# Kernel optimization log

Hardware: AMD Instinct MI355X
Metric: run time of the kernel (lower is better)

The kernel has to match this reference:

```python
import jax, jax.numpy as jnp
import numpy as np

VOCAB = 50265
D = 768
N_NEW = 200          # rows in new_embedding before zero-pad row
N_NODES = N_NEW - 1  # GAT operates on new_emb[1:-1]
N_EDGES = 1024
B, S = 8, 4096
LEAKY_SLOPE = 0.2


def setup_inputs() -> dict:
    key = jax.random.key(0)
    ks = jax.random.split(key, 7)
    x = jax.random.randint(ks[0], (B, S), 0, VOCAB + N_NEW, dtype=jnp.int32)
    orig_emb = jax.random.normal(ks[1], (VOCAB, D), dtype=jnp.float32) * 0.02
    new_emb = jax.random.normal(ks[2], (N_NEW + 1, D), dtype=jnp.float32) * 0.02
    new_emb = new_emb.at[0].set(0.0)  # prepended zero/pad row, as in __init__
    W = jax.random.normal(ks[3], (D, D), dtype=jnp.float32) * (1.0 / np.sqrt(D))
    a_src = jax.random.normal(ks[4], (D,), dtype=jnp.float32) * 0.1
    a_dst = jax.random.normal(ks[5], (D,), dtype=jnp.float32) * 0.1
    edge_index = jax.random.randint(ks[6], (2, N_EDGES), 0, N_NODES, dtype=jnp.int32)
    return {"x": x, "orig_emb": orig_emb, "new_emb": new_emb, "W": W,
            "a_src": a_src, "a_dst": a_dst, "edge_index": edge_index}


def _gat(feats, W, a_src, a_dst, edge_index):
    # Single-layer GAT over the label graph (edge list form, no dense NxN).
    h = feats @ W                                   # [N, D]
    src, dst = edge_index[0], edge_index[1]
    e = jax.nn.leaky_relu(h[src] @ a_src + h[dst] @ a_dst, LEAKY_SLOPE)  # [E]
    m = jax.ops.segment_max(e, dst, num_segments=N_NODES)               # stable softmax
    ex = jnp.exp(e - m[dst])
    denom = jax.ops.segment_sum(ex, dst, num_segments=N_NODES)
    alpha = ex / jnp.maximum(denom[dst], 1e-9)                          # [E]
    agg = jax.ops.segment_sum(alpha[:, None] * h[src], dst, num_segments=N_NODES)
    return jax.nn.elu(agg) + feats                  # residual, [N, D]


def reference(x, orig_emb, new_emb, W, a_src, a_dst, edge_index):
    # weight(): graph-encode new rows 1:-1, re-append last row, concat with vocab table
    node_feats = new_emb[1:-1]                      # [N_NODES, D]
    graph_feats = _gat(node_feats, W, a_src, a_dst, edge_index)
    table = jnp.concatenate([orig_emb, graph_feats, new_emb[-1:]], axis=0)  # [VOCAB+N_NEW, D]
    # F.embedding(x, table, padding_idx) forward is a plain gather
    return table[x]                                 # [B, S, D]
```

## Files before the change

kernel.cpp:

```cpp
#include <hip/hip_runtime.h>
#include <math.h>

#define VOCAB   50265
#define D       768
#define N_NEW   200
#define N_NODES 199
#define N_EDGES 1024
#define LEAKY   0.2f

typedef float f4 __attribute__((ext_vector_type(4)));

#define ROW_T 4
#define KC    8
#define KLEN  96
#define NROWT 50
#define NCH   (KC * 3)
#define NB_GEMM (NROWT * 3 * KC)

__global__ __launch_bounds__(256) void hybrid_kernel(
    const int* __restrict__ x, const float* __restrict__ orig_emb,
    const float* __restrict__ new_emb, const float* __restrict__ W,
    const float* __restrict__ a_src, const float* __restrict__ a_dst,
    float* __restrict__ partial, float* __restrict__ svp, float* __restrict__ dvp,
    float* __restrict__ out, int* __restrict__ gcnt, int* __restrict__ glist,
    int ntok)
{
    const int tid = threadIdx.x;
    const int bid = blockIdx.x;

    if (bid < NB_GEMM) {
        __shared__ float fts[ROW_T][KLEN];
        __shared__ float rS[ROW_T][4], rD[ROW_T][4];
        const int rowt = bid % NROWT;
        const int colt = (bid / NROWT) % 3;
        const int kc   = bid / (NROWT * 3);
        const int row0 = rowt * ROW_T;
        const int col  = colt * 256 + tid;
        const int k0   = kc * KLEN;
        const int lane = tid & 63, wid = tid >> 6;

        for (int i = tid; i < ROW_T * KLEN; i += 256) {
            int r  = i / KLEN;
            int kk = i - r * KLEN;
            int row = row0 + r;
            fts[r][kk] = (row < N_NODES) ? new_emb[(size_t)(1 + row) * D + k0 + kk] : 0.f;
        }
        __syncthreads();

        float acc[ROW_T] = {0.f, 0.f, 0.f, 0.f};
        #pragma unroll 4
        for (int kk = 0; kk < KLEN; ++kk) {
            float w = W[(size_t)(k0 + kk) * D + col];
            #pragma unroll
            for (int r = 0; r < ROW_T; ++r)
                acc[r] = fmaf(fts[r][kk], w, acc[r]);
        }

        const size_t base = ((size_t)kc * N_NODES) * D + col;
        #pragma unroll
        for (int r = 0; r < ROW_T; ++r)
            if (row0 + r < N_NODES) partial[base + (size_t)(row0 + r) * D] = acc[r];

        const float as = a_src[col];
        const float ad = a_dst[col];
        #pragma unroll
        for (int r = 0; r < ROW_T; ++r) {
            float ps = acc[r] * as;
            float pd = acc[r] * ad;
            #pragma unroll
            for (int off = 32; off; off >>= 1) {
                ps += __shfl_down(ps, off, 64);
                pd += __shfl_down(pd, off, 64);
            }
            if (lane == 0) { rS[r][wid] = ps; rD[r][wid] = pd; }
        }
        __syncthreads();
        if (tid < ROW_T) {
            const int row = row0 + tid;
            if (row < N_NODES) {
                const int slot = row * NCH + kc * 3 + colt;
                svp[slot] = rS[tid][0] + rS[tid][1] + rS[tid][2] + rS[tid][3];
                dvp[slot] = rD[tid][0] + rD[tid][1] + rD[tid][2] + rD[tid][3];
            }
        }
        return;
    }

    const int token = (bid - NB_GEMM) * 4 + (tid >> 6);
    if (token >= ntok) return;
    const int lane = tid & 63;
    const int idx = x[token];

    if (idx >= VOCAB && idx < VOCAB + N_NODES) {
        if (lane == 0) {
            int pos = atomicAdd(gcnt, 1);
            glist[pos] = token;
        }
        return;
    }

    const f4* src = (idx < VOCAB)
        ? (const f4*)(orig_emb + (size_t)idx * D)
        : (const f4*)(new_emb + (size_t)N_NEW * D);

    f4* dst = (f4*)(out + (size_t)token * D);
    f4 v0 = src[lane];
    f4 v1 = src[lane + 64];
    f4 v2 = src[lane + 128];
    __builtin_nontemporal_store(v0, &dst[lane]);
    __builtin_nontemporal_store(v1, &dst[lane + 64]);
    __builtin_nontemporal_store(v2, &dst[lane + 128]);
}

__global__ __launch_bounds__(256) void softagg_kernel(
    const int* __restrict__ edge_index, const float* __restrict__ svp,
    const float* __restrict__ dvp, const float* __restrict__ partial,
    const float* __restrict__ new_emb, float* __restrict__ gfeats)
{
    __shared__ float sv_l[N_NODES], dv_l[N_NODES];
    __shared__ float e[N_EDGES];
    __shared__ short ssrc[N_EDGES];
    __shared__ short ml[N_EDGES];
    __shared__ int   wsum[4];
    __shared__ int   s_total;
    const int n   = blockIdx.x;
    const int tid = threadIdx.x;
    const int lane = tid & 63, wid = tid >> 6;

    for (int i = tid; i < N_NODES; i += 256) {
        float s = 0.f, d = 0.f;
        #pragma unroll
        for (int q = 0; q < NCH; ++q) {
            s += svp[i * NCH + q];
            d += dvp[i * NCH + q];
        }
        sv_l[i] = s;
        dv_l[i] = d;
    }
    __syncthreads();

    const int4 se = ((const int4*)edge_index)[tid];
    const int4 de = ((const int4*)(edge_index + N_EDGES))[tid];
    const int srcs[4] = { se.x, se.y, se.z, se.w };
    const int dsts[4] = { de.x, de.y, de.z, de.w };

    int mycnt = 0;
    #pragma unroll
    for (int j = 0; j < 4; ++j) {
        const int k = 4 * tid + j;
        float ev = sv_l[srcs[j]] + dv_l[dsts[j]];
        e[k] = ev > 0.f ? ev : LEAKY * ev;
        ssrc[k] = (short)srcs[j];
        if (dsts[j] == n) ++mycnt;
    }

    int pre = mycnt;
    #pragma unroll
    for (int off = 1; off < 64; off <<= 1) {
        int v = __shfl_up(pre, off, 64);
        if (lane >= off) pre += v;
    }
    if (lane == 63) wsum[wid] = pre;
    __syncthreads();
    int woff = 0;
    for (int w = 0; w < wid; ++w) woff += wsum[w];
    int base = woff + pre - mycnt;
    #pragma unroll
    for (int j = 0; j < 4; ++j) {
        if (dsts[j] == n) ml[base++] = (short)(4 * tid + j);
    }
    if (tid == 255) s_total = woff + pre;
    __syncthreads();

    const int c = s_total;

    float mx = -INFINITY;
    for (int p = 0; p < c; ++p) mx = fmaxf(mx, e[ml[p]]);
    float dn = 0.f;
    for (int p = 0; p < c; ++p) dn += expf(e[ml[p]] - mx);
    const float inv = 1.f / fmaxf(dn, 1e-9f);

    const size_t kcstride = (size_t)N_NODES * D;
    float a0 = 0.f, a1 = 0.f, a2 = 0.f;
    for (int p = 0; p < c; ++p) {
        const int k = ml[p];
        const float a = expf(e[k] - mx) * inv;
        const float* pb = partial + (size_t)ssrc[k] * D;
        float h0 = 0.f, h1 = 0.f, h2 = 0.f;
        #pragma unroll
        for (int q = 0; q < KC; ++q) {
            h0 += pb[q * kcstride + tid];
            h1 += pb[q * kcstride + tid + 256];
            h2 += pb[q * kcstride + tid + 512];
        }
        a0 = fmaf(a, h0, a0);
        a1 = fmaf(a, h1, a1);
        a2 = fmaf(a, h2, a2);
    }
    const float* f = new_emb + (size_t)(1 + n) * D;
    float e0 = a0 > 0.f ? a0 : expf(a0) - 1.f;
    float e1 = a1 > 0.f ? a1 : expf(a1) - 1.f;
    float e2 = a2 > 0.f ? a2 : expf(a2) - 1.f;
    gfeats[(size_t)n * D + tid]       = e0 + f[tid];
    gfeats[(size_t)n * D + tid + 256] = e1 + f[tid + 256];
    gfeats[(size_t)n * D + tid + 512] = e2 + f[tid + 512];
}

#define FIX_BLOCKS 64
__global__ __launch_bounds__(256) void fixup_kernel(
    const int* __restrict__ x, const float* __restrict__ gfeats,
    const int* __restrict__ gcnt, const int* __restrict__ glist,
    float* __restrict__ out)
{
    const int lane = threadIdx.x & 63;
    const int wid  = threadIdx.x >> 6;
    const int cnt  = *gcnt;

    for (int i = blockIdx.x * 4 + wid; i < cnt; i += FIX_BLOCKS * 4) {
        const int token = glist[i];
        const int n = x[token] - VOCAB;
        const f4* src = (const f4*)(gfeats + (size_t)n * D);
        f4* dst = (f4*)(out + (size_t)token * D);
        f4 v0 = src[lane];
        f4 v1 = src[lane + 64];
        f4 v2 = src[lane + 128];
        __builtin_nontemporal_store(v0, &dst[lane]);
        __builtin_nontemporal_store(v1, &dst[lane + 64]);
        __builtin_nontemporal_store(v2, &dst[lane + 128]);
    }
}

extern "C" void kernel_launch(void* const* d_in, const int* in_sizes, int n_in,
                              void* d_out, int out_size, void* d_ws, size_t ws_size,
                              hipStream_t stream) {
    const int*   x        = (const int*)  d_in[0];
    const float* orig_emb = (const float*)d_in[1];
    const float* new_emb  = (const float*)d_in[2];
    const float* W        = (const float*)d_in[3];
    const float* a_src    = (const float*)d_in[4];
    const float* a_dst    = (const float*)d_in[5];
    const int*   edge_idx = (const int*)  d_in[6];
    float* out = (float*)d_out;

    int*   gcnt    = (int*)d_ws;
    float* partial = (float*)((char*)d_ws + 256);
    float* svp     = partial + (size_t)KC * N_NODES * D;
    float* dvp     = svp + N_NODES * NCH;
    float* gfeats  = dvp + N_NODES * NCH;
    int*   glist   = (int*)(gfeats + (size_t)N_NODES * D);

    const int ntok = in_sizes[0];
    const int nblocks = NB_GEMM + (ntok + 3) / 4;

    hipMemsetAsync(gcnt, 0, 16, stream);
    hybrid_kernel<<<nblocks, 256, 0, stream>>>(
        x, orig_emb, new_emb, W, a_src, a_dst,
        partial, svp, dvp, out, gcnt, glist, ntok);
    softagg_kernel<<<N_NODES, 256, 0, stream>>>(
        edge_idx, svp, dvp, partial, new_emb, gfeats);
    fixup_kernel<<<FIX_BLOCKS, 256, 0, stream>>>(
        x, gfeats, gcnt, glist, out);
}
```

Before: 56.88 us.

## Vectorize GEMM tiles over full row width and fuse fixup into softmax aggregation

```diff
diff --git a/kernel.cpp b/kernel.cpp
--- a/kernel.cpp
+++ b/kernel.cpp
@@ -14,8 +14,7 @@
 #define KC    8
 #define KLEN  96
 #define NROWT 50
-#define NCH   (KC * 3)
-#define NB_GEMM (NROWT * 3 * KC)
+#define NB_GEMM (NROWT * KC)
 
 __global__ __launch_bounds__(256) void hybrid_kernel(
     const int* __restrict__ x, const float* __restrict__ orig_emb,
@@ -30,12 +29,10 @@
 
     if (bid < NB_GEMM) {
         __shared__ float fts[ROW_T][KLEN];
-        __shared__ float rS[ROW_T][4], rD[ROW_T][4];
+        __shared__ float rS[ROW_T][3], rD[ROW_T][3];
         const int rowt = bid % NROWT;
-        const int colt = (bid / NROWT) % 3;
-        const int kc   = bid / (NROWT * 3);
+        const int kc   = bid / NROWT;
         const int row0 = rowt * ROW_T;
-        const int col  = colt * 256 + tid;
         const int k0   = kc * KLEN;
         const int lane = tid & 63, wid = tid >> 6;
 
@@ -47,40 +44,47 @@
         }
         __syncthreads();
 
-        float acc[ROW_T] = {0.f, 0.f, 0.f, 0.f};
-        #pragma unroll 4
-        for (int kk = 0; kk < KLEN; ++kk) {
-            float w = W[(size_t)(k0 + kk) * D + col];
+        if (tid < 192) {
+            const f4* Wf4 = (const f4*)W;
+            f4 acc[ROW_T];
             #pragma unroll
-            for (int r = 0; r < ROW_T; ++r)
-                acc[r] = fmaf(fts[r][kk], w, acc[r]);
-        }
-
-        const size_t base = ((size_t)kc * N_NODES) * D + col;
-        #pragma unroll
-        for (int r = 0; r < ROW_T; ++r)
-            if (row0 + r < N_NODES) partial[base + (size_t)(row0 + r) * D] = acc[r];
-
-        const float as = a_src[col];
-        const float ad = a_dst[col];
-        #pragma unroll
-        for (int r = 0; r < ROW_T; ++r) {
-            float ps = acc[r] * as;
-            float pd = acc[r] * ad;
+            for (int r = 0; r < ROW_T; ++r) acc[r] = (f4){0.f, 0.f, 0.f, 0.f};
+
+            #pragma unroll 4
+            for (int kk = 0; kk < KLEN; ++kk) {
+                const f4 w = Wf4[(size_t)(k0 + kk) * 192 + tid];
+                #pragma unroll
+                for (int r = 0; r < ROW_T; ++r)
+                    acc[r] += fts[r][kk] * w;
+            }
+
             #pragma unroll
-            for (int off = 32; off; off >>= 1) {
-                ps += __shfl_down(ps, off, 64);
-                pd += __shfl_down(pd, off, 64);
-            }
-            if (lane == 0) { rS[r][wid] = ps; rD[r][wid] = pd; }
+            for (int r = 0; r < ROW_T; ++r) {
+                const int row = row0 + r;
+                if (row < N_NODES)
+                    ((f4*)(partial + ((size_t)kc * N_NODES + row) * D))[tid] = acc[r];
+            }
+
+            const f4 as = ((const f4*)a_src)[tid];
+            const f4 ad = ((const f4*)a_dst)[tid];
+            #pragma unroll
+            for (int r = 0; r < ROW_T; ++r) {
+                float ps = acc[r].x * as.x + acc[r].y * as.y + acc[r].z * as.z + acc[r].w * as.w;
+                float pd = acc[r].x * ad.x + acc[r].y * ad.y + acc[r].z * ad.z + acc[r].w * ad.w;
+                #pragma unroll
+                for (int off = 32; off; off >>= 1) {
+                    ps += __shfl_down(ps, off, 64);
+                    pd += __shfl_down(pd, off, 64);
+                }
+                if (lane == 0) { rS[r][wid] = ps; rD[r][wid] = pd; }
+            }
         }
         __syncthreads();
         if (tid < ROW_T) {
             const int row = row0 + tid;
             if (row < N_NODES) {
-                const int slot = row * NCH + kc * 3 + colt;
-                svp[slot] = rS[tid][0] + rS[tid][1] + rS[tid][2] + rS[tid][3];
-                dvp[slot] = rD[tid][0] + rD[tid][1] + rD[tid][2] + rD[tid][3];
+                svp[row * KC + kc] = rS[tid][0] + rS[tid][1] + rS[tid][2];
+                dvp[row * KC + kc] = rD[tid][0] + rD[tid][1] + rD[tid][2];
             }
         }
         return;
@@ -112,10 +116,12 @@
     __builtin_nontemporal_store(v2, &dst[lane + 128]);
 }
 
-__global__ __launch_bounds__(256) void softagg_kernel(
-    const int* __restrict__ edge_index, const float* __restrict__ svp,
-    const float* __restrict__ dvp, const float* __restrict__ partial,
-    const float* __restrict__ new_emb, float* __restrict__ gfeats)
+__global__ __launch_bounds__(256) void softagg_out_kernel(
+    const int* __restrict__ x, const int* __restrict__ edge_index,
+    const float* __restrict__ svp, const float* __restrict__ dvp,
+    const float* __restrict__ partial, const float* __restrict__ new_emb,
+    const int* __restrict__ gcnt, const int* __restrict__ glist,
+    float* __restrict__ out)
 {
     __shared__ float sv_l[N_NODES], dv_l[N_NODES];
     __shared__ float e[N_EDGES];
@@ -123,6 +129,8 @@
     __shared__ short ml[N_EDGES];
     __shared__ int   wsum[4];
     __shared__ int   s_total;
+    __shared__ int   t_tok[256];
+    __shared__ short t_node[256];
     const int n   = blockIdx.x;
     const int tid = threadIdx.x;
     const int lane = tid & 63, wid = tid >> 6;
@@ -130,9 +138,9 @@
     for (int i = tid; i < N_NODES; i += 256) {
         float s = 0.f, d = 0.f;
         #pragma unroll
-        for (int q = 0; q < NCH; ++q) {
-            s += svp[i * NCH + q];
-            d += dvp[i * NCH + q];
+        for (int q = 0; q < KC; ++q) {
+            s += svp[i * KC + q];
+            d += dvp[i * KC + q];
         }
         sv_l[i] = s;
         dv_l[i] = d;
@@ -198,35 +206,28 @@
         a2 = fmaf(a, h2, a2);
     }
     const float* f = new_emb + (size_t)(1 + n) * D;
-    float e0 = a0 > 0.f ? a0 : expf(a0) - 1.f;
-    float e1 = a1 > 0.f ? a1 : expf(a1) - 1.f;
-    float e2 = a2 > 0.f ? a2 : expf(a2) - 1.f;
-    gfeats[(size_t)n * D + tid]       = e0 + f[tid];
-    gfeats[(size_t)n * D + tid + 256] = e1 + f[tid + 256];
-    gfeats[(size_t)n * D + tid + 512] = e2 + f[tid + 512];
-}
-
-#define FIX_BLOCKS 64
-__global__ __launch_bounds__(256) void fixup_kernel(
-    const int* __restrict__ x, const float* __restrict__ gfeats,
-    const int* __restrict__ gcnt, const int* __restrict__ glist,
-    float* __restrict__ out)
-{
-    const int lane = threadIdx.x & 63;
-    const int wid  = threadIdx.x >> 6;
-    const int cnt  = *gcnt;
-
-    for (int i = blockIdx.x * 4 + wid; i < cnt; i += FIX_BLOCKS * 4) {
-        const int token = glist[i];
-        const int n = x[token] - VOCAB;
-        const f4* src = (const f4*)(gfeats + (size_t)n * D);
-        f4* dst = (f4*)(out + (size_t)token * D);
-        f4 v0 = src[lane];
-        f4 v1 = src[lane + 64];
-        f4 v2 = src[lane + 128];
-        __builtin_nontemporal_store(v0, &dst[lane]);
-        __builtin_nontemporal_store(v1, &dst[lane + 64]);
-        __builtin_nontemporal_store(v2, &dst[lane + 128]);
+    const float e0 = (a0 > 0.f ? a0 : expf(a0) - 1.f) + f[tid];
+    const float e1 = (a1 > 0.f ? a1 : expf(a1) - 1.f) + f[tid + 256];
+    const float e2 = (a2 > 0.f ? a2 : expf(a2) - 1.f) + f[tid + 512];
+
+    const int cnt = *gcnt;
+    for (int b = 0; b < cnt; b += 256) {
+        const int p = b + tid;
+        int tok = -1, nd = -1;
+        if (p < cnt) { tok = glist[p]; nd = x[tok] - VOCAB; }
+        t_tok[tid] = tok;
+        t_node[tid] = (short)nd;
+        __syncthreads();
+        const int lim = min(256, cnt - b);
+        for (int q = 0; q < lim; ++q) {
+            if ((int)t_node[q] == n) {
+                float* o = out + (size_t)t_tok[q] * D;
+                o[tid]       = e0;
+                o[tid + 256] = e1;
+                o[tid + 512] = e2;
+            }
+        }
+        __syncthreads();
     }
 }
 
@@ -245,9 +246,8 @@
     int*   gcnt    = (int*)d_ws;
     float* partial = (float*)((char*)d_ws + 256);
     float* svp     = partial + (size_t)KC * N_NODES * D;
-    float* dvp     = svp + N_NODES * NCH;
-    float* gfeats  = dvp + N_NODES * NCH;
-    int*   glist   = (int*)(gfeats + (size_t)N_NODES * D);
+    float* dvp     = svp + N_NODES * KC;
+    int*   glist   = (int*)(dvp + N_NODES * KC);
 
     const int ntok = in_sizes[0];
     const int nblocks = NB_GEMM + (ntok + 3) / 4;
@@ -256,8 +256,6 @@
     hybrid_kernel<<<nblocks, 256, 0, stream>>>(
         x, orig_emb, new_emb, W, a_src, a_dst,
         partial, svp, dvp, out, gcnt, glist, ntok);
-    softagg_kernel<<<N_NODES, 256, 0, stream>>>(
-        edge_idx, svp, dvp, partial, new_emb, gfeats);
-    fixup_kernel<<<FIX_BLOCKS, 256, 0, stream>>>(
-        x, gfeats, gcnt, glist, out);
+    softagg_out_kernel<<<N_NODES, 256, 0, stream>>>(
+        x, edge_idx, svp, dvp, partial, new_emb, gcnt, glist, out);
 }
```

Measured after the change: 61.67 us. 8.4% more time.
